# Optimization experiments

Hardware: AMD Instinct MI355X
Metric: run time of the kernel (lower is better)

Reference implementation:

```python
import jax, jax.numpy as jnp
import numpy as np

TOP_K = 2


def layer_norm(x, g, b, eps=1e-5):
    m = jnp.mean(x, axis=-1, keepdims=True)
    v = jnp.mean((x - m) ** 2, axis=-1, keepdims=True)
    return (x - m) * jax.lax.rsqrt(v + eps) * g + b


def setup_inputs() -> dict:
    key = jax.random.key(0)
    ks = jax.random.split(key, 6)
    B, P, D, E, K = 8, 1024, 1024, 8, TOP_K
    x = jax.random.normal(ks[0], (B, P, D), dtype=jnp.float32)
    noise = jax.random.normal(ks[1], (B * P * K, D), dtype=jnp.float32) * 1e-5
    Wg = jax.random.normal(ks[2], (D, E), dtype=jnp.float32) * 0.02
    bg = jnp.zeros((E,), dtype=jnp.float32)
    W1 = jax.random.normal(ks[3], (E, D, D), dtype=jnp.float32) * 0.02
    b1 = jnp.zeros((E, D), dtype=jnp.float32)
    W2 = jax.random.normal(ks[4], (E, D, D), dtype=jnp.float32) * 0.02
    b2 = jnp.zeros((E, D), dtype=jnp.float32)
    ln_g = jnp.ones((E, D), dtype=jnp.float32)
    ln_b = jnp.zeros((E, D), dtype=jnp.float32)
    gn_g = jnp.ones((D,), dtype=jnp.float32)
    gn_b = jnp.zeros((D,), dtype=jnp.float32)
    return {"x": x, "noise": noise, "Wg": Wg, "bg": bg, "W1": W1, "b1": b1,
            "W2": W2, "b2": b2, "ln_g": ln_g, "ln_b": ln_b, "gn_g": gn_g, "gn_b": gn_b}


def reference(x, noise, Wg, bg, W1, b1, W2, b2, ln_g, ln_b, gn_g, gn_b):
    # Eval-mode forward of Allocator (aux_loss == 0, not returned).
    B, P, D = x.shape
    E = Wg.shape[1]
    K = TOP_K
    N = B * P
    logits = jnp.einsum('bpd,de->bpe', x, Wg) + bg          # [B,P,E]
    probs = jax.nn.softmax(logits, axis=-1).reshape(N, E)
    _topk_probs, topk_idx = jax.lax.top_k(probs, K)          # probs unused in eval combine
    flat_idx = topk_idx.reshape(-1)                          # [N*K]
    sample_idx = jnp.repeat(jnp.arange(N), K)                # [N*K]
    batch_idx = sample_idx // P                              # [N*K]
    xg = x.reshape(N, D)[sample_idx] + noise                 # [N*K, D] gathered token copies
    sums = []
    for e in range(E):  # fixed small expert loop
        h = jax.nn.gelu(xg @ W1[e] + b1[e], approximate=False)
        y = h @ W2[e] + b2[e] + xg                           # Mlp + residual
        y = layer_norm(y, ln_g[e], ln_b[e])                  # Expert.norm
        m = (flat_idx == e)[:, None]
        # one_hot(batch_idx).T @ masked_output == per-batch segment sum (unweighted)
        sums.append(jax.ops.segment_sum(jnp.where(m, y, 0.0), batch_idx, num_segments=B))
    out = jnp.stack(sums, axis=0).transpose(1, 0, 2)         # [B, E, D]
    return layer_norm(out, gn_g, gn_b)
```

## Files before the change

kernel.cpp:

```cpp
#include <hip/hip_runtime.h>
#include <hip/hip_bf16.h>
#include <math.h>

#define D 1024
#define NTOK 8192
#define NSLOT 16384
#define NGRP 64
#define MAXTILE 136

typedef short bf16x8 __attribute__((ext_vector_type(8)));
typedef float floatx4 __attribute__((ext_vector_type(4)));

__device__ __forceinline__ unsigned short f2bf(float f) {
    __hip_bfloat16 h = __float2bfloat16(f);
    return *reinterpret_cast<unsigned short*>(&h);
}
__device__ __forceinline__ float bf2f(unsigned short u) {
    unsigned int v = ((unsigned int)u) << 16;
    return __uint_as_float(v);
}

__device__ __forceinline__ void load_lds16(const void* g, void* l) {
    __builtin_amdgcn_global_load_lds(
        (const __attribute__((address_space(1))) unsigned int*)g,
        (__attribute__((address_space(3))) unsigned int*)l, 16, 0, 0);
}

__global__ void zero_kernel(int* __restrict__ grp_cnt, float* __restrict__ S) {
    int i = blockIdx.x * 256 + threadIdx.x;
    if (i < NGRP) grp_cnt[i] = 0;
    if (i < 64 * D) S[i] = 0.f;
}

__global__ void route_kernel(const float* __restrict__ x, const float* __restrict__ Wg,
                             const float* __restrict__ bg, int* __restrict__ slot_e,
                             int* __restrict__ grp_cnt) {
    int wave = threadIdx.x >> 6;
    int lane = threadIdx.x & 63;
    int tok = blockIdx.x * 4 + wave;
    const float* xr = x + (size_t)tok * D;
    float acc[8] = {0.f,0.f,0.f,0.f,0.f,0.f,0.f,0.f};
    for (int k = lane; k < D; k += 64) {
        float xv = xr[k];
        const float4* w4 = reinterpret_cast<const float4*>(Wg + k * 8);
        float4 a = w4[0], b = w4[1];
        acc[0] += xv * a.x; acc[1] += xv * a.y; acc[2] += xv * a.z; acc[3] += xv * a.w;
        acc[4] += xv * b.x; acc[5] += xv * b.y; acc[6] += xv * b.z; acc[7] += xv * b.w;
    }
#pragma unroll
    for (int e = 0; e < 8; e++) {
#pragma unroll
        for (int off = 32; off > 0; off >>= 1)
            acc[e] += __shfl_xor(acc[e], off, 64);
    }
    if (lane == 0) {
        float lg[8];
#pragma unroll
        for (int e = 0; e < 8; e++) lg[e] = acc[e] + bg[e];
        int e1 = 0; float b1v = lg[0];
#pragma unroll
        for (int e = 1; e < 8; e++) if (lg[e] > b1v) { b1v = lg[e]; e1 = e; }
        int e2 = -1; float b2v = -3.0e38f;
#pragma unroll
        for (int e = 0; e < 8; e++) { if (e == e1) continue; if (lg[e] > b2v) { b2v = lg[e]; e2 = e; } }
        int b = tok >> 10;
        slot_e[2 * tok] = e1;
        slot_e[2 * tok + 1] = e2;
        atomicAdd(&grp_cnt[e1 * 8 + b], 1);
        atomicAdd(&grp_cnt[e2 * 8 + b], 1);
    }
}

__global__ void prefix_kernel(const int* __restrict__ grp_cnt, int* __restrict__ goff,
                              int* __restrict__ cursor, int2* __restrict__ tile_tab) {
    if (threadIdx.x != 0) return;
    int s = 0;
    for (int g = 0; g < NGRP; g++) { goff[g] = s; cursor[g] = s; s += grp_cnt[g]; }
    goff[NGRP] = s;
    int t = 0;
    for (int e = 0; e < 8; e++) {
        int cnt = goff[e * 8 + 8] - goff[e * 8];
        for (int m0 = 0; m0 < cnt; m0 += 128) tile_tab[t++] = make_int2(e, m0);
    }
    for (; t < MAXTILE; t++) tile_tab[t] = make_int2(-1, 0);
}

__global__ void build_xg_kernel(const float* __restrict__ x, const float* __restrict__ noise,
                                const int* __restrict__ slot_e, int* __restrict__ cursor,
                                unsigned short* __restrict__ xg) {
    int wave = threadIdx.x >> 6;
    int lane = threadIdx.x & 63;
    int slot = blockIdx.x * 4 + wave;
    int e = slot_e[slot];
    int b = slot >> 11;
    int row = 0;
    if (lane == 0) row = atomicAdd(&cursor[e * 8 + b], 1);
    row = __shfl(row, 0, 64);
    int tok = slot >> 1;
    const float4* xr = reinterpret_cast<const float4*>(x + (size_t)tok * D);
    const float4* nr = reinterpret_cast<const float4*>(noise + (size_t)slot * D);
    ushort4* og = reinterpret_cast<ushort4*>(xg + (size_t)row * D);
    for (int i = lane; i < D / 4; i += 64) {
        float4 a = xr[i], n = nr[i];
        ushort4 o;
        o.x = f2bf(a.x + n.x); o.y = f2bf(a.y + n.y);
        o.z = f2bf(a.z + n.z); o.w = f2bf(a.w + n.w);
        og[i] = o;
    }
}

__global__ void wconv_kernel(const float* __restrict__ W1, const float* __restrict__ W2,
                             unsigned short* __restrict__ W1t, unsigned short* __restrict__ W2t) {
    __shared__ unsigned short t[128][65];
    int z = blockIdx.z;
    int mat = z & 1, e = z >> 1;
    const float* src = (mat ? W2 : W1) + (size_t)e * D * D;
    unsigned short* dst = (mat ? W2t : W1t) + (size_t)e * D * D;
    int k0 = blockIdx.x * 128, n0 = blockIdx.y * 64;
    int tx = threadIdx.x & 63, ty = threadIdx.x >> 6;
    for (int r = ty; r < 128; r += 4)
        t[r][tx] = f2bf(src[(size_t)(k0 + r) * D + n0 + tx]);
    __syncthreads();
    for (int j = ty; j < 64; j += 4) {
        ushort2 o;
        o.x = t[2 * tx][j];
        o.y = t[2 * tx + 1][j];
        *reinterpret_cast<ushort2*>(dst + (size_t)(n0 + j) * D + k0 + 2 * tx) = o;
    }
}

template <int MODE>
__global__ __launch_bounds__(256)
void gemm_kernel(const unsigned short* __restrict__ A,
                 const unsigned short* __restrict__ Wt,
                 const float* __restrict__ bias,
                 const unsigned short* __restrict__ xg,
                 const int2* __restrict__ tile_tab,
                 const int* __restrict__ goff,
                 unsigned short* __restrict__ Hout) {
    __shared__ unsigned short As[128 * 32];
    __shared__ unsigned short Bs[128 * 32];

    int2 tt = tile_tab[blockIdx.x];
    int e = tt.x;
    if (e < 0) return;
    int m0 = tt.y;
    int rowBase = goff[e * 8];
    int cnt = goff[e * 8 + 8] - rowBase;
    int n0 = blockIdx.y * 128;

    const unsigned short* Ab = A + (size_t)rowBase * D;
    const unsigned short* Bb = Wt + (size_t)e * D * D + (size_t)n0 * D;

    int tid = threadIdx.x;
    int lane = tid & 63, wave = tid >> 6;
    int wm = wave >> 1, wn = wave & 1;
    int lr = lane & 15, quad = lane >> 4;
    int l2 = lane >> 2, l4 = lane & 3;

    floatx4 acc[4][4] = {};

    for (int k0 = 0; k0 < D; k0 += 32) {
#pragma unroll
        for (int c = 0; c < 2; c++) {
            int chunk = wave * 2 + c;
            int row = m0 + chunk * 16 + l2;
            row = min(row, cnt - 1);
            const unsigned short* gp = Ab + ((size_t)row << 10) + k0 + l4 * 8;
            unsigned short* lp = As + chunk * 512 + lane * 8;
            load_lds16(gp, lp);
        }
#pragma unroll
        for (int c = 0; c < 2; c++) {
            int chunk = wave * 2 + c;
            int brow = chunk * 16 + l2;
            const unsigned short* gp = Bb + ((size_t)brow << 10) + k0 + l4 * 8;
            unsigned short* lp = Bs + chunk * 512 + lane * 8;
            load_lds16(gp, lp);
        }
        __syncthreads();

        bf16x8 af[4], bfr[4];
#pragma unroll
        for (int i = 0; i < 4; i++)
            af[i] = *reinterpret_cast<const bf16x8*>(As + (wm * 64 + i * 16 + lr) * 32 + quad * 8);
#pragma unroll
        for (int j = 0; j < 4; j++)
            bfr[j] = *reinterpret_cast<const bf16x8*>(Bs + (wn * 64 + j * 16 + lr) * 32 + quad * 8);
#pragma unroll
        for (int i = 0; i < 4; i++)
#pragma unroll
            for (int j = 0; j < 4; j++)
                acc[i][j] = __builtin_amdgcn_mfma_f32_16x16x32_bf16(af[i], bfr[j], acc[i][j], 0, 0, 0);
        __syncthreads();
    }

#pragma unroll
    for (int i = 0; i < 4; i++) {
        int rowb = m0 + wm * 64 + i * 16 + quad * 4;
#pragma unroll
        for (int j = 0; j < 4; j++) {
            int col = n0 + wn * 64 + j * 16 + lr;
            float bia = bias[e * D + col];
#pragma unroll
            for (int r = 0; r < 4; r++) {
                int rr = rowb + r;
                if (rr < cnt) {
                    float v = acc[i][j][r] + bia;
                    size_t idx = (size_t)(rowBase + rr) * D + col;
                    if (MODE == 0) {
                        float g = 0.5f * v * (1.0f + erff(v * 0.70710678118654752f));
                        Hout[idx] = f2bf(g);
                    } else {
                        v += bf2f(xg[idx]);
                        Hout[idx] = f2bf(v);
                    }
                }
            }
        }
    }
}

__global__ void lnsum_kernel(const unsigned short* __restrict__ ybf,
                             const int* __restrict__ goff, float* __restrict__ S) {
    int grp = blockIdx.x, chunk = blockIdx.y;
    int r0 = goff[grp] + chunk * 64;
    int r1 = min(goff[grp + 1], r0 + 64);
    if (r0 >= r1) return;
    __shared__ float part[D];
    for (int i = threadIdx.x; i < D; i += 256) part[i] = 0.f;
    __syncthreads();

    int wave = threadIdx.x >> 6, lane = threadIdx.x & 63;
    float p[16] = {0.f};
    for (int r = r0 + wave; r < r1; r += 4) {
        const unsigned short* row = ybf + ((size_t)r << 10);
        float v[16];
        float s = 0.f, sq = 0.f;
#pragma unroll
        for (int c = 0; c < 4; c++) {
            ushort4 u = *reinterpret_cast<const ushort4*>(row + c * 256 + lane * 4);
            float a = bf2f(u.x), b = bf2f(u.y), cc = bf2f(u.z), d = bf2f(u.w);
            v[c * 4 + 0] = a; v[c * 4 + 1] = b; v[c * 4 + 2] = cc; v[c * 4 + 3] = d;
            s += a + b + cc + d;
            sq += a * a + b * b + cc * cc + d * d;
        }
#pragma unroll
        for (int off = 32; off > 0; off >>= 1) {
            s += __shfl_xor(s, off, 64);
            sq += __shfl_xor(sq, off, 64);
        }
        float m = s * (1.f / 1024.f);
        float rs = rsqrtf(sq * (1.f / 1024.f) - m * m + 1e-5f);
#pragma unroll
        for (int c = 0; c < 16; c++) p[c] += (v[c] - m) * rs;
    }
#pragma unroll
    for (int c = 0; c < 4; c++)
#pragma unroll
        for (int q = 0; q < 4; q++)
            atomicAdd(&part[c * 256 + lane * 4 + q], p[c * 4 + q]);
    __syncthreads();

    int e = grp >> 3, b = grp & 7;
    float* Sp = S + (size_t)(b * 8 + e) * D;
    for (int i = threadIdx.x; i < D; i += 256)
        atomicAdd(&Sp[i], part[i]);
}

__global__ void finalize_kernel(const float* __restrict__ S, const int* __restrict__ goff,
                                const float* __restrict__ ln_g, const float* __restrict__ ln_b,
                                const float* __restrict__ gn_g, const float* __restrict__ gn_b,
                                float* __restrict__ out) {
    int be = blockIdx.x;
    int b = be >> 3, e = be & 7;
    int grp = e * 8 + b;
    float cnt = (float)(goff[grp + 1] - goff[grp]);
    int tid = threadIdx.x;
    __shared__ float red[8];
    float val[4];
    float s = 0.f, sq = 0.f;
#pragma unroll
    for (int c = 0; c < 4; c++) {
        int d = tid * 4 + c;
        float v = S[(size_t)be * D + d] * ln_g[e * D + d] + cnt * ln_b[e * D + d];
        val[c] = v; s += v; sq += v * v;
    }
#pragma unroll
    for (int off = 32; off > 0; off >>= 1) {
        s += __shfl_xor(s, off, 64);
        sq += __shfl_xor(sq, off, 64);
    }
    int wave = tid >> 6, lane = tid & 63;
    if (lane == 0) { red[wave] = s; red[4 + wave] = sq; }
    __syncthreads();
    float ts = red[0] + red[1] + red[2] + red[3];
    float tq = red[4] + red[5] + red[6] + red[7];
    float m = ts / 1024.f;
    float var = tq / 1024.f - m * m;
    float rstd = rsqrtf(var + 1e-5f);
#pragma unroll
    for (int c = 0; c < 4; c++) {
        int d = tid * 4 + c;
        out[(size_t)be * D + d] = (val[c] - m) * rstd * gn_g[d] + gn_b[d];
    }
}

extern "C" void kernel_launch(void* const* d_in, const int* in_sizes, int n_in,
                              void* d_out, int out_size, void* d_ws, size_t ws_size,
                              hipStream_t stream) {
    const float* x     = (const float*)d_in[0];
    const float* noise = (const float*)d_in[1];
    const float* Wg    = (const float*)d_in[2];
    const float* bg    = (const float*)d_in[3];
    const float* W1    = (const float*)d_in[4];
    const float* b1    = (const float*)d_in[5];
    const float* W2    = (const float*)d_in[6];
    const float* b2    = (const float*)d_in[7];
    const float* ln_g  = (const float*)d_in[8];
    const float* ln_b  = (const float*)d_in[9];
    const float* gn_g  = (const float*)d_in[10];
    const float* gn_b  = (const float*)d_in[11];
    float* out = (float*)d_out;

    char* ws = (char*)d_ws;
    size_t off = 0;
    unsigned short* xg   = (unsigned short*)(ws + off); off += (size_t)NSLOT * D * 2;
    unsigned short* hb   = (unsigned short*)(ws + off); off += (size_t)NSLOT * D * 2;
    unsigned short* ybf  = (unsigned short*)(ws + off); off += (size_t)NSLOT * D * 2;
    unsigned short* W1t  = (unsigned short*)(ws + off); off += (size_t)8 * D * D * 2;
    unsigned short* W2t  = (unsigned short*)(ws + off); off += (size_t)8 * D * D * 2;
    int* slot_e          = (int*)(ws + off);            off += (size_t)NSLOT * 4;
    int* grp_cnt         = (int*)(ws + off);            off += 256;
    int* goff            = (int*)(ws + off);            off += 512;
    int* cursor          = (int*)(ws + off);            off += 256;
    int2* tile_tab       = (int2*)(ws + off);           off += MAXTILE * 8;
    float* S             = (float*)(ws + off);          off += (size_t)64 * D * 4;

    zero_kernel<<<256, 256, 0, stream>>>(grp_cnt, S);
    route_kernel<<<NTOK / 4, 256, 0, stream>>>(x, Wg, bg, slot_e, grp_cnt);
    prefix_kernel<<<1, 64, 0, stream>>>(grp_cnt, goff, cursor, tile_tab);
    wconv_kernel<<<dim3(8, 16, 16), 256, 0, stream>>>(W1, W2, W1t, W2t);
    build_xg_kernel<<<NSLOT / 4, 256, 0, stream>>>(x, noise, slot_e, cursor, xg);
    gemm_kernel<0><<<dim3(MAXTILE, 8), 256, 0, stream>>>(xg, W1t, b1, xg, tile_tab, goff, hb);
    gemm_kernel<1><<<dim3(MAXTILE, 8), 256, 0, stream>>>(hb, W2t, b2, xg, tile_tab, goff, ybf);
    lnsum_kernel<<<dim3(64, 16), 256, 0, stream>>>(ybf, goff, S);
    finalize_kernel<<<64, 256, 0, stream>>>(S, goff, ln_g, ln_b, gn_g, gn_b, out);
}
```

Measured before the change: 542.2 us.

## Double-buffer GEMM LDS loads, shrink N tile, and retile weight layout

Expert GEMMs now double-buffer the A and B LDS tiles so the next k-slice load is issued before the MFMAs on the current one. The N tile shrinks from 128 to 64 and the grid is reordered so N-blocks vary fastest, which doubles the block count and improves weight reuse in cache across neighbouring blocks. Weight conversion writes a k-blocked [K/8][N][8] bf16 layout without an LDS transpose, so each B load row is contiguous. The smaller tile lowers arithmetic intensity per block and re-reads A twice as often.

```diff
diff --git a/kernel.cpp b/kernel.cpp
--- a/kernel.cpp
+++ b/kernel.cpp
@@ -111,21 +111,28 @@
 
 __global__ void wconv_kernel(const float* __restrict__ W1, const float* __restrict__ W2,
                              unsigned short* __restrict__ W1t, unsigned short* __restrict__ W2t) {
-    __shared__ unsigned short t[128][65];
-    int z = blockIdx.z;
+    int z = blockIdx.y;
     int mat = z & 1, e = z >> 1;
     const float* src = (mat ? W2 : W1) + (size_t)e * D * D;
     unsigned short* dst = (mat ? W2t : W1t) + (size_t)e * D * D;
-    int k0 = blockIdx.x * 128, n0 = blockIdx.y * 64;
-    int tx = threadIdx.x & 63, ty = threadIdx.x >> 6;
-    for (int r = ty; r < 128; r += 4)
-        t[r][tx] = f2bf(src[(size_t)(k0 + r) * D + n0 + tx]);
-    __syncthreads();
-    for (int j = ty; j < 64; j += 4) {
-        ushort2 o;
-        o.x = t[2 * tx][j];
-        o.y = t[2 * tx + 1][j];
-        *reinterpret_cast<ushort2*>(dst + (size_t)(n0 + j) * D + k0 + 2 * tx) = o;
+    int kc = blockIdx.x;
+    int tid = threadIdx.x;
+#pragma unroll
+    for (int p = 0; p < 4; p++) {
+        int n = p * 256 + tid;
+#pragma unroll
+        for (int kb = 0; kb < 8; kb++) {
+            int kbase = kc * 64 + kb * 8;
+            unsigned int w[4];
+#pragma unroll
+            for (int kk = 0; kk < 4; kk++) {
+                unsigned short lo = f2bf(src[(size_t)(kbase + 2 * kk) * D + n]);
+                unsigned short hi = f2bf(src[(size_t)(kbase + 2 * kk + 1) * D + n]);
+                w[kk] = (unsigned int)lo | ((unsigned int)hi << 16);
+            }
+            uint4 o = make_uint4(w[0], w[1], w[2], w[3]);
+            *reinterpret_cast<uint4*>(dst + (size_t)(kbase >> 3) * (D * 8) + (size_t)n * 8) = o;
+        }
     }
 }
 
@@ -138,19 +145,16 @@
                  const int2* __restrict__ tile_tab,
                  const int* __restrict__ goff,
                  unsigned short* __restrict__ Hout) {
-    __shared__ unsigned short As[128 * 32];
-    __shared__ unsigned short Bs[128 * 32];
-
-    int2 tt = tile_tab[blockIdx.x];
+    __shared__ unsigned short As[2][128 * 32];
+    __shared__ unsigned short Bs[2][64 * 32];
+
+    int2 tt = tile_tab[blockIdx.y];
     int e = tt.x;
     if (e < 0) return;
     int m0 = tt.y;
     int rowBase = goff[e * 8];
     int cnt = goff[e * 8 + 8] - rowBase;
-    int n0 = blockIdx.y * 128;
-
-    const unsigned short* Ab = A + (size_t)rowBase * D;
-    const unsigned short* Bb = Wt + (size_t)e * D * D + (size_t)n0 * D;
+    int n0 = blockIdx.x * 64;
 
     int tid = threadIdx.x;
     int lane = tid & 63, wave = tid >> 6;
@@ -158,49 +162,77 @@
     int lr = lane & 15, quad = lane >> 4;
     int l2 = lane >> 2, l4 = lane & 3;
 
-    floatx4 acc[4][4] = {};
-
-    for (int k0 = 0; k0 < D; k0 += 32) {
-#pragma unroll
-        for (int c = 0; c < 2; c++) {
-            int chunk = wave * 2 + c;
-            int row = m0 + chunk * 16 + l2;
-            row = min(row, cnt - 1);
-            const unsigned short* gp = Ab + ((size_t)row << 10) + k0 + l4 * 8;
-            unsigned short* lp = As + chunk * 512 + lane * 8;
-            load_lds16(gp, lp);
-        }
-#pragma unroll
-        for (int c = 0; c < 2; c++) {
-            int chunk = wave * 2 + c;
-            int brow = chunk * 16 + l2;
-            const unsigned short* gp = Bb + ((size_t)brow << 10) + k0 + l4 * 8;
-            unsigned short* lp = Bs + chunk * 512 + lane * 8;
-            load_lds16(gp, lp);
-        }
+    int arow0 = min(m0 + (wave * 2 + 0) * 16 + l2, cnt - 1);
+    int arow1 = min(m0 + (wave * 2 + 1) * 16 + l2, cnt - 1);
+    const unsigned short* ap0 = A + ((size_t)(rowBase + arow0) << 10) + l4 * 8;
+    const unsigned short* ap1 = A + ((size_t)(rowBase + arow1) << 10) + l4 * 8;
+    const unsigned short* bp = Wt + (size_t)e * D * D
+                               + (size_t)l4 * (D * 8)
+                               + (size_t)(n0 + wave * 16 + l2) * 8;
+
+    unsigned short* a_dst0[2] = { &As[0][(wave * 2 + 0) * 512 + lane * 8],
+                                  &As[1][(wave * 2 + 0) * 512 + lane * 8] };
+    unsigned short* a_dst1[2] = { &As[0][(wave * 2 + 1) * 512 + lane * 8],
+                                  &As[1][(wave * 2 + 1) * 512 + lane * 8] };
+    unsigned short* b_dst[2]  = { &Bs[0][wave * 512 + lane * 8],
+                                  &Bs[1][wave * 512 + lane * 8] };
+
+    const unsigned short* a_frag = &As[0][(wm * 64 + lr) * 32 + quad * 8];
+    const unsigned short* b_frag = &Bs[0][(wn * 32 + lr) * 32 + quad * 8];
+
+    floatx4 acc[4][2] = {};
+
+    load_lds16(ap0, a_dst0[0]); load_lds16(ap1, a_dst1[0]); load_lds16(bp, b_dst[0]);
+    ap0 += 32; ap1 += 32; bp += 4 * D * 8;
+
+#pragma unroll 1
+    for (int k0 = 0; k0 < D; k0 += 64) {
         __syncthreads();
-
-        bf16x8 af[4], bfr[4];
-#pragma unroll
-        for (int i = 0; i < 4; i++)
-            af[i] = *reinterpret_cast<const bf16x8*>(As + (wm * 64 + i * 16 + lr) * 32 + quad * 8);
-#pragma unroll
-        for (int j = 0; j < 4; j++)
-            bfr[j] = *reinterpret_cast<const bf16x8*>(Bs + (wn * 64 + j * 16 + lr) * 32 + quad * 8);
-#pragma unroll
-        for (int i = 0; i < 4; i++)
-#pragma unroll
-            for (int j = 0; j < 4; j++)
-                acc[i][j] = __builtin_amdgcn_mfma_f32_16x16x32_bf16(af[i], bfr[j], acc[i][j], 0, 0, 0);
+        if (k0 + 32 < D) {
+            load_lds16(ap0, a_dst0[1]); load_lds16(ap1, a_dst1[1]); load_lds16(bp, b_dst[1]);
+            ap0 += 32; ap1 += 32; bp += 4 * D * 8;
+        }
+        {
+            bf16x8 af[4], bfr[2];
+#pragma unroll
+            for (int i = 0; i < 4; i++)
+                af[i] = *reinterpret_cast<const bf16x8*>(a_frag + i * 512);
+#pragma unroll
+            for (int j = 0; j < 2; j++)
+                bfr[j] = *reinterpret_cast<const bf16x8*>(b_frag + j * 512);
+#pragma unroll
+            for (int i = 0; i < 4; i++)
+#pragma unroll
+                for (int j = 0; j < 2; j++)
+                    acc[i][j] = __builtin_amdgcn_mfma_f32_16x16x32_bf16(af[i], bfr[j], acc[i][j], 0, 0, 0);
+        }
         __syncthreads();
+        if (k0 + 64 < D) {
+            load_lds16(ap0, a_dst0[0]); load_lds16(ap1, a_dst1[0]); load_lds16(bp, b_dst[0]);
+            ap0 += 32; ap1 += 32; bp += 4 * D * 8;
+        }
+        {
+            bf16x8 af[4], bfr[2];
+#pragma unroll
+            for (int i = 0; i < 4; i++)
+                af[i] = *reinterpret_cast<const bf16x8*>(a_frag + 4096 + i * 512);
+#pragma unroll
+            for (int j = 0; j < 2; j++)
+                bfr[j] = *reinterpret_cast<const bf16x8*>(b_frag + 2048 + j * 512);
+#pragma unroll
+            for (int i = 0; i < 4; i++)
+#pragma unroll
+                for (int j = 0; j < 2; j++)
+                    acc[i][j] = __builtin_amdgcn_mfma_f32_16x16x32_bf16(af[i], bfr[j], acc[i][j], 0, 0, 0);
+        }
     }
 
 #pragma unroll
     for (int i = 0; i < 4; i++) {
         int rowb = m0 + wm * 64 + i * 16 + quad * 4;
 #pragma unroll
-        for (int j = 0; j < 4; j++) {
-            int col = n0 + wn * 64 + j * 16 + lr;
+        for (int j = 0; j < 2; j++) {
+            int col = n0 + wn * 32 + j * 16 + lr;
             float bia = bias[e * D + col];
 #pragma unroll
             for (int r = 0; r < 4; r++) {
@@ -340,10 +372,10 @@
     zero_kernel<<<256, 256, 0, stream>>>(grp_cnt, S);
     route_kernel<<<NTOK / 4, 256, 0, stream>>>(x, Wg, bg, slot_e, grp_cnt);
     prefix_kernel<<<1, 64, 0, stream>>>(grp_cnt, goff, cursor, tile_tab);
-    wconv_kernel<<<dim3(8, 16, 16), 256, 0, stream>>>(W1, W2, W1t, W2t);
+    wconv_kernel<<<dim3(16, 16), 256, 0, stream>>>(W1, W2, W1t, W2t);
     build_xg_kernel<<<NSLOT / 4, 256, 0, stream>>>(x, noise, slot_e, cursor, xg);
-    gemm_kernel<0><<<dim3(MAXTILE, 8), 256, 0, stream>>>(xg, W1t, b1, xg, tile_tab, goff, hb);
-    gemm_kernel<1><<<dim3(MAXTILE, 8), 256, 0, stream>>>(hb, W2t, b2, xg, tile_tab, goff, ybf);
+    gemm_kernel<0><<<dim3(16, MAXTILE), 256, 0, stream>>>(xg, W1t, b1, xg, tile_tab, goff, hb);
+    gemm_kernel<1><<<dim3(16, MAXTILE), 256, 0, stream>>>(hb, W2t, b2, xg, tile_tab, goff, ybf);
     lnsum_kernel<<<dim3(64, 16), 256, 0, stream>>>(ybf, goff, S);
     finalize_kernel<<<64, 256, 0, stream>>>(S, goff, ln_g, ln_b, gn_g, gn_b, out);
 }
```

Result: slower. 587.2 us (+8.3%).
